# Performance work log

Measured on AMD Instinct MI355X. Metric: run time of the kernel, lower is better.

## Reference

```python
import jax, jax.numpy as jnp
import numpy as np


def setup_inputs() -> dict:
    key = jax.random.key(0)
    ks = jax.random.split(key, 5)
    B, Td, Te, D, U = 8, 64, 1024, 256, 128
    scale = 1.0 / np.sqrt(D)
    return {
        "decoder_output": jax.random.normal(ks[0], (B, Td, D), jnp.float32),
        "encoder_output": jax.random.normal(ks[1], (B, Te, D), jnp.float32),
        "W1": jax.random.normal(ks[2], (D, U), jnp.float32) * scale,
        "b1": jnp.zeros((U,), jnp.float32),
        "W2": jax.random.normal(ks[3], (D, U), jnp.float32) * scale,
        "b2": jnp.zeros((U,), jnp.float32),
        "V": jax.random.normal(ks[4], (U, 1), jnp.float32) * (1.0 / np.sqrt(U)),
        "bV": jnp.zeros((1,), jnp.float32),
    }


def reference(decoder_output, encoder_output, W1, b1, W2, b2, V, bV):
    # Original loops over decoder timesteps (state unused) -> fully vectorized.
    # w_enc: [B,Te,U] computed ONCE (original wastefully recomputes per step;
    # math is identical).
    w_enc = jnp.einsum("bsd,du->bsu", encoder_output, W1) + b1
    w_dec = jnp.einsum("btd,du->btu", decoder_output, W2) + b2
    # additive score: [B,Td,Te]
    score = (
        jnp.einsum("btsu,u->bts", jnp.tanh(w_enc[:, None, :, :] + w_dec[:, :, None, :]), V[:, 0])
        + bV[0]
    )
    attn = jax.nn.softmax(score, axis=-1)  # softmax over encoder time
    context = jnp.einsum("bts,bsd->btd", attn, encoder_output)  # [B,Td,D]
    return context
```

## Files before the change

### kernel.cpp

```cpp
#include <hip/hip_runtime.h>
#include <math.h>

#define NB   8
#define TD   64
#define TE   1024
#define DDIM 256
#define UDIM 128

__device__ __forceinline__ float rcp_fast(float x) {
    return __builtin_amdgcn_rcpf(x);
}

__global__ __launch_bounds__(256) void k_compute_E(
    const float* __restrict__ enc, const float* __restrict__ dec,
    const float* __restrict__ W1, const float* __restrict__ b1,
    const float* __restrict__ W2, const float* __restrict__ b2,
    float* __restrict__ E_enc, float* __restrict__ E_dec)
{
    __shared__ alignas(16) float ldsT[DDIM][20];

    const int blk = blockIdx.x;
    const float *W, *bias, *in;
    float *out;
    if (blk < 512) {
        in   = enc + (size_t)blk * 16 * DDIM;
        W    = W1;  bias = b1;
        out  = E_enc + (size_t)blk * 16 * UDIM;
    } else {
        const int bd = blk - 512;
        in   = dec + (size_t)bd * 16 * DDIM;
        W    = W2;  bias = b2;
        out  = E_dec + (size_t)bd * 16 * UDIM;
    }

    const int tid = threadIdx.x;
    for (int i = tid; i < 16 * DDIM; i += 256) {
        const int r = i >> 8;
        const int d = i & 255;
        ldsT[d][r] = in[i];
    }
    __syncthreads();

    const int u0 = (tid & 63) * 2;
    const int r0 = (tid >> 6) * 4;

    float acc[4][2];
    #pragma unroll
    for (int r = 0; r < 4; ++r) { acc[r][0] = 0.f; acc[r][1] = 0.f; }

    #pragma unroll 4
    for (int d = 0; d < DDIM; ++d) {
        const float2 w2 = *(const float2*)(W + d * UDIM + u0);
        const float4 a4 = *(const float4*)(&ldsT[d][r0]);
        acc[0][0] = fmaf(a4.x, w2.x, acc[0][0]); acc[0][1] = fmaf(a4.x, w2.y, acc[0][1]);
        acc[1][0] = fmaf(a4.y, w2.x, acc[1][0]); acc[1][1] = fmaf(a4.y, w2.y, acc[1][1]);
        acc[2][0] = fmaf(a4.z, w2.x, acc[2][0]); acc[2][1] = fmaf(a4.z, w2.y, acc[2][1]);
        acc[3][0] = fmaf(a4.w, w2.x, acc[3][0]); acc[3][1] = fmaf(a4.w, w2.y, acc[3][1]);
    }

    const float k2l2e = 2.0f * 1.4426950408889634f;
    const float bb0 = bias[u0], bb1 = bias[u0 + 1];
    #pragma unroll
    for (int r = 0; r < 4; ++r) {
        const float e0 = exp2f((acc[r][0] + bb0) * k2l2e);
        const float e1 = exp2f((acc[r][1] + bb1) * k2l2e);
        *(float2*)(out + (size_t)(r0 + r) * UDIM + u0) = make_float2(e0, e1);
    }
}

__global__ __launch_bounds__(1024) void k_fused(
    const float* __restrict__ E_enc, const float* __restrict__ E_dec,
    const float* __restrict__ V, const float* __restrict__ enc,
    float* __restrict__ out)
{
    __shared__ alignas(16) float pa[TE];
    __shared__ alignas(16) float pb[TE];
    __shared__ alignas(16) float red[8][2][DDIM];
    __shared__ float redm[16][2];
    __shared__ float reds[16][2];

    const int blk = blockIdx.x;
    const int b   = blk >> 5;
    const int t0  = (blk & 31) * 2;
    const int tid = threadIdx.x;

    const float* er0 = E_dec + (size_t)(b * TD + t0) * UDIM;
    const float* er1 = er0 + UDIM;

    const int s = tid;
    const float* erow = E_enc + (size_t)(b * TE + s) * UDIM;

    float acc0 = 0.f, acc1 = 0.f;
    #pragma unroll 8
    for (int u = 0; u < UDIM; u += 4) {
        const float4 e  = *(const float4*)(erow + u);
        const float4 a0 = *(const float4*)(er0 + u);
        const float4 a1 = *(const float4*)(er1 + u);
        const float4 vv = *(const float4*)(V + u);
        acc0 = fmaf(vv.x, rcp_fast(fmaf(e.x, a0.x, 1.f)), acc0);
        acc1 = fmaf(vv.x, rcp_fast(fmaf(e.x, a1.x, 1.f)), acc1);
        acc0 = fmaf(vv.y, rcp_fast(fmaf(e.y, a0.y, 1.f)), acc0);
        acc1 = fmaf(vv.y, rcp_fast(fmaf(e.y, a1.y, 1.f)), acc1);
        acc0 = fmaf(vv.z, rcp_fast(fmaf(e.z, a0.z, 1.f)), acc0);
        acc1 = fmaf(vv.z, rcp_fast(fmaf(e.z, a1.z, 1.f)), acc1);
        acc0 = fmaf(vv.w, rcp_fast(fmaf(e.w, a0.w, 1.f)), acc0);
        acc1 = fmaf(vv.w, rcp_fast(fmaf(e.w, a1.w, 1.f)), acc1);
    }
    acc0 *= -2.0f;
    acc1 *= -2.0f;

    float m0 = acc0, m1 = acc1;
    #pragma unroll
    for (int off = 32; off; off >>= 1) {
        m0 = fmaxf(m0, __shfl_xor(m0, off));
        m1 = fmaxf(m1, __shfl_xor(m1, off));
    }
    const int wv = tid >> 6;
    if ((tid & 63) == 0) { redm[wv][0] = m0; redm[wv][1] = m1; }
    __syncthreads();
    float gm0 = -3.4e38f, gm1 = -3.4e38f;
    #pragma unroll
    for (int i = 0; i < 16; ++i) {
        gm0 = fmaxf(gm0, redm[i][0]);
        gm1 = fmaxf(gm1, redm[i][1]);
    }

    const float p0 = __expf(acc0 - gm0);
    const float p1 = __expf(acc1 - gm1);

    float s0 = p0, s1 = p1;
    #pragma unroll
    for (int off = 32; off; off >>= 1) {
        s0 += __shfl_xor(s0, off);
        s1 += __shfl_xor(s1, off);
    }
    if ((tid & 63) == 0) { reds[wv][0] = s0; reds[wv][1] = s1; }
    __syncthreads();
    float gs0 = 0.f, gs1 = 0.f;
    #pragma unroll
    for (int i = 0; i < 16; ++i) { gs0 += reds[i][0]; gs1 += reds[i][1]; }

    pa[s] = p0 * rcp_fast(gs0);
    pb[s] = p1 * rcp_fast(gs1);
    __syncthreads();

    const int dp = tid & 127;
    const int d0 = dp * 2;
    const int sq = tid >> 7;
    const float* ebase = enc + ((size_t)(b * TE + sq * 128)) * DDIM + d0;

    float c00 = 0.f, c01 = 0.f, c10 = 0.f, c11 = 0.f;
    #pragma unroll 4
    for (int ss = 0; ss < 128; ++ss) {
        const float a0 = pa[sq * 128 + ss];
        const float a1 = pb[sq * 128 + ss];
        const float2 e = *(const float2*)(ebase + (size_t)ss * DDIM);
        c00 = fmaf(a0, e.x, c00);
        c01 = fmaf(a0, e.y, c01);
        c10 = fmaf(a1, e.x, c10);
        c11 = fmaf(a1, e.y, c11);
    }
    *(float2*)(&red[sq][0][d0]) = make_float2(c00, c01);
    *(float2*)(&red[sq][1][d0]) = make_float2(c10, c11);
    __syncthreads();

    if (tid < 512) {
        const int t = tid >> 8;
        const int d = tid & 255;
        float r = 0.f;
        #pragma unroll
        for (int q = 0; q < 8; ++q) r += red[q][t][d];
        out[(size_t)(b * TD + t0 + t) * DDIM + d] = r;
    }
}

extern "C" void kernel_launch(void* const* d_in, const int* in_sizes, int n_in,
                              void* d_out, int out_size, void* d_ws, size_t ws_size,
                              hipStream_t stream) {
    const float* dec = (const float*)d_in[0];
    const float* enc = (const float*)d_in[1];
    const float* W1  = (const float*)d_in[2];
    const float* b1  = (const float*)d_in[3];
    const float* W2  = (const float*)d_in[4];
    const float* b2  = (const float*)d_in[5];
    const float* V   = (const float*)d_in[6];

    float* ws    = (float*)d_ws;
    float* E_enc = ws;
    float* E_dec = E_enc + (size_t)NB * TE * UDIM;

    k_compute_E<<<544, 256,  0, stream>>>(enc, dec, W1, b1, W2, b2, E_enc, E_dec);
    k_fused    <<<256, 1024, 0, stream>>>(E_enc, E_dec, V, enc, (float*)d_out);
}
```

Baseline: 131.1 us.

## Split attention over encoder chunks with flash-style partial softmax and combine kernel

Restructures the fused score/softmax/context kernel so each block handles 16 decoder steps over a 128-long encoder chunk, instead of 2 decoder steps over the full encoder length. Each block writes partial max/sum and partial context, and a new combine kernel merges them with rescaling. The encoder projection is stored in a float4-interleaved transposed layout so loads across encoder positions coalesce, and each encoder tile is reused across more decoder rows. The cost is an extra kernel launch and a global round trip for the partial results.

```diff
diff --git a/kernel.cpp b/kernel.cpp
--- a/kernel.cpp
+++ b/kernel.cpp
@@ -6,6 +6,10 @@
 #define TE   1024
 #define DDIM 256
 #define UDIM 128
+#define NSG  8
+#define SLEN 128
+#define NTG  4
+#define TLEN 16
 
 __device__ __forceinline__ float rcp_fast(float x) {
     return __builtin_amdgcn_rcpf(x);
@@ -15,163 +19,195 @@
     const float* __restrict__ enc, const float* __restrict__ dec,
     const float* __restrict__ W1, const float* __restrict__ b1,
     const float* __restrict__ W2, const float* __restrict__ b2,
-    float* __restrict__ E_enc, float* __restrict__ E_dec)
+    float* __restrict__ E_T, float* __restrict__ E_dec)
 {
     __shared__ alignas(16) float ldsT[DDIM][20];
 
     const int blk = blockIdx.x;
-    const float *W, *bias, *in;
-    float *out;
+    const int tid = threadIdx.x;
+    const float k2l2e = 2.0f * 1.4426950408889634f;
+
     if (blk < 512) {
-        in   = enc + (size_t)blk * 16 * DDIM;
-        W    = W1;  bias = b1;
-        out  = E_enc + (size_t)blk * 16 * UDIM;
+        const int b    = blk >> 6;
+        const int row0 = (blk & 63) * 16;
+        const float* in = enc + ((size_t)b * TE + row0) * DDIM;
+
+        for (int i = tid; i < 16 * DDIM; i += 256) {
+            ldsT[i & 255][i >> 8] = in[i];
+        }
+        __syncthreads();
+
+        const int uq = tid >> 3;
+        const int rr = (tid & 7) * 2;
+        const int u0 = uq * 4;
+
+        float4 A0 = make_float4(0.f, 0.f, 0.f, 0.f);
+        float4 A1 = make_float4(0.f, 0.f, 0.f, 0.f);
+
+        #pragma unroll 8
+        for (int d = 0; d < DDIM; ++d) {
+            const float4 w4 = *(const float4*)(W1 + d * UDIM + u0);
+            const float2 a2 = *(const float2*)(&ldsT[d][rr]);
+            A0.x = fmaf(a2.x, w4.x, A0.x); A1.x = fmaf(a2.y, w4.x, A1.x);
+            A0.y = fmaf(a2.x, w4.y, A0.y); A1.y = fmaf(a2.y, w4.y, A1.y);
+            A0.z = fmaf(a2.x, w4.z, A0.z); A1.z = fmaf(a2.y, w4.z, A1.z);
+            A0.w = fmaf(a2.x, w4.w, A0.w); A1.w = fmaf(a2.y, w4.w, A1.w);
+        }
+
+        const float4 bb = *(const float4*)(b1 + u0);
+        float4 q0, q1;
+        q0.x = exp2f((A0.x + bb.x) * k2l2e);  q1.x = exp2f((A1.x + bb.x) * k2l2e);
+        q0.y = exp2f((A0.y + bb.y) * k2l2e);  q1.y = exp2f((A1.y + bb.y) * k2l2e);
+        q0.z = exp2f((A0.z + bb.z) * k2l2e);  q1.z = exp2f((A1.z + bb.z) * k2l2e);
+        q0.w = exp2f((A0.w + bb.w) * k2l2e);  q1.w = exp2f((A1.w + bb.w) * k2l2e);
+
+        float4* E_T4 = (float4*)E_T;
+        const size_t qbase = ((size_t)b * 32 + uq) * TE + row0 + rr;
+        E_T4[qbase]     = q0;
+        E_T4[qbase + 1] = q1;
     } else {
         const int bd = blk - 512;
-        in   = dec + (size_t)bd * 16 * DDIM;
-        W    = W2;  bias = b2;
-        out  = E_dec + (size_t)bd * 16 * UDIM;
-    }
-
+        const float* in = dec + (size_t)bd * 16 * DDIM;
+        float* out = E_dec + (size_t)bd * 16 * UDIM;
+
+        for (int i = tid; i < 16 * DDIM; i += 256) {
+            ldsT[i & 255][i >> 8] = in[i];
+        }
+        __syncthreads();
+
+        const int u0 = (tid & 63) * 2;
+        const int r0 = (tid >> 6) * 4;
+
+        float acc[4][2];
+        #pragma unroll
+        for (int r = 0; r < 4; ++r) { acc[r][0] = 0.f; acc[r][1] = 0.f; }
+
+        #pragma unroll 8
+        for (int d = 0; d < DDIM; ++d) {
+            const float2 w2 = *(const float2*)(W2 + d * UDIM + u0);
+            const float4 a4 = *(const float4*)(&ldsT[d][r0]);
+            acc[0][0] = fmaf(a4.x, w2.x, acc[0][0]); acc[0][1] = fmaf(a4.x, w2.y, acc[0][1]);
+            acc[1][0] = fmaf(a4.y, w2.x, acc[1][0]); acc[1][1] = fmaf(a4.y, w2.y, acc[1][1]);
+            acc[2][0] = fmaf(a4.z, w2.x, acc[2][0]); acc[2][1] = fmaf(a4.z, w2.y, acc[2][1]);
+            acc[3][0] = fmaf(a4.w, w2.x, acc[3][0]); acc[3][1] = fmaf(a4.w, w2.y, acc[3][1]);
+        }
+
+        const float bb0 = b2[u0], bb1 = b2[u0 + 1];
+        #pragma unroll
+        for (int r = 0; r < 4; ++r) {
+            const float e0 = exp2f((acc[r][0] + bb0) * k2l2e);
+            const float e1 = exp2f((acc[r][1] + bb1) * k2l2e);
+            *(float2*)(out + (size_t)(r0 + r) * UDIM + u0) = make_float2(e0, e1);
+        }
+    }
+}
+
+__global__ __launch_bounds__(1024) void k_fused2(
+    const float* __restrict__ E_T, const float* __restrict__ E_dec,
+    const float* __restrict__ V, const float* __restrict__ enc,
+    float2* __restrict__ ml, float* __restrict__ part)
+{
+    __shared__ float sc[TLEN][SLEN];
+
+    const int blk = blockIdx.x;
+    const int b   = blk >> 5;
+    const int tg  = (blk >> 3) & 3;
+    const int sg  = blk & 7;
     const int tid = threadIdx.x;
-    for (int i = tid; i < 16 * DDIM; i += 256) {
-        const int r = i >> 8;
-        const int d = i & 255;
-        ldsT[d][r] = in[i];
-    }
+
+    const int sl = tid & 127;
+    const int th = __builtin_amdgcn_readfirstlane(tid >> 7);
+    const int sglob = sg * SLEN + sl;
+
+    const float4* e4  = (const float4*)E_T + (size_t)b * 32 * TE + sglob;
+    const float*  er0 = E_dec + (size_t)(b * TD + tg * TLEN + th) * UDIM;
+    const float*  er1 = er0 + 8 * UDIM;
+
+    float acc0 = 0.f, acc1 = 0.f;
+    #pragma unroll 8
+    for (int uq = 0; uq < 32; ++uq) {
+        const float4 e = e4[(size_t)uq * TE];
+        const int u0 = uq * 4;
+        const float v0 = V[u0], v1 = V[u0+1], v2 = V[u0+2], v3 = V[u0+3];
+        acc0 = fmaf(v0, rcp_fast(fmaf(e.x, er0[u0  ], 1.f)), acc0);
+        acc1 = fmaf(v0, rcp_fast(fmaf(e.x, er1[u0  ], 1.f)), acc1);
+        acc0 = fmaf(v1, rcp_fast(fmaf(e.y, er0[u0+1], 1.f)), acc0);
+        acc1 = fmaf(v1, rcp_fast(fmaf(e.y, er1[u0+1], 1.f)), acc1);
+        acc0 = fmaf(v2, rcp_fast(fmaf(e.z, er0[u0+2], 1.f)), acc0);
+        acc1 = fmaf(v2, rcp_fast(fmaf(e.z, er1[u0+2], 1.f)), acc1);
+        acc0 = fmaf(v3, rcp_fast(fmaf(e.w, er0[u0+3], 1.f)), acc0);
+        acc1 = fmaf(v3, rcp_fast(fmaf(e.w, er1[u0+3], 1.f)), acc1);
+    }
+    sc[th][sl]     = -2.0f * acc0;
+    sc[th + 8][sl] = -2.0f * acc1;
     __syncthreads();
 
-    const int u0 = (tid & 63) * 2;
-    const int r0 = (tid >> 6) * 4;
-
-    float acc[4][2];
-    #pragma unroll
-    for (int r = 0; r < 4; ++r) { acc[r][0] = 0.f; acc[r][1] = 0.f; }
-
+    const int tw = __builtin_amdgcn_readfirstlane(tid >> 6);
+    const int ln = tid & 63;
+    const float v0s = sc[tw][ln];
+    const float v1s = sc[tw][ln + 64];
+    float m = fmaxf(v0s, v1s);
+    #pragma unroll
+    for (int off = 32; off; off >>= 1) m = fmaxf(m, __shfl_xor(m, off));
+    const float p0 = __expf(v0s - m);
+    const float p1 = __expf(v1s - m);
+    float l = p0 + p1;
+    #pragma unroll
+    for (int off = 32; off; off >>= 1) l += __shfl_xor(l, off);
+    sc[tw][ln]      = p0;
+    sc[tw][ln + 64] = p1;
+    if (ln == 0)
+        ml[(size_t)(b * TD + tg * TLEN + tw) * NSG + sg] = make_float2(m, l);
+    __syncthreads();
+
+    const int dp = tid & 127;  const int d0 = dp * 2;
+    const int tq = __builtin_amdgcn_readfirstlane(tid >> 7);
+    const float* eb = enc + ((size_t)(b * TE + sg * SLEN)) * DDIM + d0;
+
+    float c00 = 0.f, c01 = 0.f, c10 = 0.f, c11 = 0.f;
     #pragma unroll 4
-    for (int d = 0; d < DDIM; ++d) {
-        const float2 w2 = *(const float2*)(W + d * UDIM + u0);
-        const float4 a4 = *(const float4*)(&ldsT[d][r0]);
-        acc[0][0] = fmaf(a4.x, w2.x, acc[0][0]); acc[0][1] = fmaf(a4.x, w2.y, acc[0][1]);
-        acc[1][0] = fmaf(a4.y, w2.x, acc[1][0]); acc[1][1] = fmaf(a4.y, w2.y, acc[1][1]);
-        acc[2][0] = fmaf(a4.z, w2.x, acc[2][0]); acc[2][1] = fmaf(a4.z, w2.y, acc[2][1]);
-        acc[3][0] = fmaf(a4.w, w2.x, acc[3][0]); acc[3][1] = fmaf(a4.w, w2.y, acc[3][1]);
-    }
-
-    const float k2l2e = 2.0f * 1.4426950408889634f;
-    const float bb0 = bias[u0], bb1 = bias[u0 + 1];
-    #pragma unroll
-    for (int r = 0; r < 4; ++r) {
-        const float e0 = exp2f((acc[r][0] + bb0) * k2l2e);
-        const float e1 = exp2f((acc[r][1] + bb1) * k2l2e);
-        *(float2*)(out + (size_t)(r0 + r) * UDIM + u0) = make_float2(e0, e1);
-    }
-}
-
-__global__ __launch_bounds__(1024) void k_fused(
-    const float* __restrict__ E_enc, const float* __restrict__ E_dec,
-    const float* __restrict__ V, const float* __restrict__ enc,
+    for (int s = 0; s < SLEN; ++s) {
+        const float2 e = *(const float2*)(eb + (size_t)s * DDIM);
+        const float a0 = sc[tq * 2][s];
+        const float a1 = sc[tq * 2 + 1][s];
+        c00 = fmaf(a0, e.x, c00); c01 = fmaf(a0, e.y, c01);
+        c10 = fmaf(a1, e.x, c10); c11 = fmaf(a1, e.y, c11);
+    }
+    const int trow = tg * TLEN + tq * 2;
+    float* pb = part + (((size_t)(b * NSG + sg) * TD) + trow) * DDIM + d0;
+    *(float2*)pb          = make_float2(c00, c01);
+    *(float2*)(pb + DDIM) = make_float2(c10, c11);
+}
+
+__global__ __launch_bounds__(256) void k_combine(
+    const float2* __restrict__ ml, const float* __restrict__ part,
     float* __restrict__ out)
 {
-    __shared__ alignas(16) float pa[TE];
-    __shared__ alignas(16) float pb[TE];
-    __shared__ alignas(16) float red[8][2][DDIM];
-    __shared__ float redm[16][2];
-    __shared__ float reds[16][2];
-
-    const int blk = blockIdx.x;
-    const int b   = blk >> 5;
-    const int t0  = (blk & 31) * 2;
-    const int tid = threadIdx.x;
-
-    const float* er0 = E_dec + (size_t)(b * TD + t0) * UDIM;
-    const float* er1 = er0 + UDIM;
-
-    const int s = tid;
-    const float* erow = E_enc + (size_t)(b * TE + s) * UDIM;
-
-    float acc0 = 0.f, acc1 = 0.f;
-    #pragma unroll 8
-    for (int u = 0; u < UDIM; u += 4) {
-        const float4 e  = *(const float4*)(erow + u);
-        const float4 a0 = *(const float4*)(er0 + u);
-        const float4 a1 = *(const float4*)(er1 + u);
-        const float4 vv = *(const float4*)(V + u);
-        acc0 = fmaf(vv.x, rcp_fast(fmaf(e.x, a0.x, 1.f)), acc0);
-        acc1 = fmaf(vv.x, rcp_fast(fmaf(e.x, a1.x, 1.f)), acc1);
-        acc0 = fmaf(vv.y, rcp_fast(fmaf(e.y, a0.y, 1.f)), acc0);
-        acc1 = fmaf(vv.y, rcp_fast(fmaf(e.y, a1.y, 1.f)), acc1);
-        acc0 = fmaf(vv.z, rcp_fast(fmaf(e.z, a0.z, 1.f)), acc0);
-        acc1 = fmaf(vv.z, rcp_fast(fmaf(e.z, a1.z, 1.f)), acc1);
-        acc0 = fmaf(vv.w, rcp_fast(fmaf(e.w, a0.w, 1.f)), acc0);
-        acc1 = fmaf(vv.w, rcp_fast(fmaf(e.w, a1.w, 1.f)), acc1);
-    }
-    acc0 *= -2.0f;
-    acc1 *= -2.0f;
-
-    float m0 = acc0, m1 = acc1;
-    #pragma unroll
-    for (int off = 32; off; off >>= 1) {
-        m0 = fmaxf(m0, __shfl_xor(m0, off));
-        m1 = fmaxf(m1, __shfl_xor(m1, off));
-    }
-    const int wv = tid >> 6;
-    if ((tid & 63) == 0) { redm[wv][0] = m0; redm[wv][1] = m1; }
-    __syncthreads();
-    float gm0 = -3.4e38f, gm1 = -3.4e38f;
-    #pragma unroll
-    for (int i = 0; i < 16; ++i) {
-        gm0 = fmaxf(gm0, redm[i][0]);
-        gm1 = fmaxf(gm1, redm[i][1]);
-    }
-
-    const float p0 = __expf(acc0 - gm0);
-    const float p1 = __expf(acc1 - gm1);
-
-    float s0 = p0, s1 = p1;
-    #pragma unroll
-    for (int off = 32; off; off >>= 1) {
-        s0 += __shfl_xor(s0, off);
-        s1 += __shfl_xor(s1, off);
-    }
-    if ((tid & 63) == 0) { reds[wv][0] = s0; reds[wv][1] = s1; }
-    __syncthreads();
-    float gs0 = 0.f, gs1 = 0.f;
-    #pragma unroll
-    for (int i = 0; i < 16; ++i) { gs0 += reds[i][0]; gs1 += reds[i][1]; }
-
-    pa[s] = p0 * rcp_fast(gs0);
-    pb[s] = p1 * rcp_fast(gs1);
-    __syncthreads();
-
-    const int dp = tid & 127;
-    const int d0 = dp * 2;
-    const int sq = tid >> 7;
-    const float* ebase = enc + ((size_t)(b * TE + sq * 128)) * DDIM + d0;
-
-    float c00 = 0.f, c01 = 0.f, c10 = 0.f, c11 = 0.f;
-    #pragma unroll 4
-    for (int ss = 0; ss < 128; ++ss) {
-        const float a0 = pa[sq * 128 + ss];
-        const float a1 = pb[sq * 128 + ss];
-        const float2 e = *(const float2*)(ebase + (size_t)ss * DDIM);
-        c00 = fmaf(a0, e.x, c00);
-        c01 = fmaf(a0, e.y, c01);
-        c10 = fmaf(a1, e.x, c10);
-        c11 = fmaf(a1, e.y, c11);
-    }
-    *(float2*)(&red[sq][0][d0]) = make_float2(c00, c01);
-    *(float2*)(&red[sq][1][d0]) = make_float2(c10, c11);
-    __syncthreads();
-
-    if (tid < 512) {
-        const int t = tid >> 8;
-        const int d = tid & 255;
-        float r = 0.f;
-        #pragma unroll
-        for (int q = 0; q < 8; ++q) r += red[q][t][d];
-        out[(size_t)(b * TD + t0 + t) * DDIM + d] = r;
-    }
+    const int bt = blockIdx.x;
+    const int d  = threadIdx.x;
+    const int b  = bt >> 6, t = bt & 63;
+
+    float2 mls[NSG];
+    float m_g = -3.4e38f;
+    #pragma unroll
+    for (int sg = 0; sg < NSG; ++sg) {
+        mls[sg] = ml[(size_t)bt * NSG + sg];
+        m_g = fmaxf(m_g, mls[sg].x);
+    }
+    float l_g = 0.f;
+    float w[NSG];
+    #pragma unroll
+    for (int sg = 0; sg < NSG; ++sg) {
+        w[sg] = __expf(mls[sg].x - m_g);
+        l_g = fmaf(mls[sg].y, w[sg], l_g);
+    }
+    const float inv = rcp_fast(l_g);
+
+    float r = 0.f;
+    #pragma unroll
+    for (int sg = 0; sg < NSG; ++sg)
+        r = fmaf(part[(((size_t)(b * NSG + sg) * TD) + t) * DDIM + d], w[sg], r);
+    out[(size_t)bt * DDIM + d] = r * inv;
 }
 
 extern "C" void kernel_launch(void* const* d_in, const int* in_sizes, int n_in,
@@ -185,10 +221,13 @@
     const float* b2  = (const float*)d_in[5];
     const float* V   = (const float*)d_in[6];
 
-    float* ws    = (float*)d_ws;
-    float* E_enc = ws;
-    float* E_dec = E_enc + (size_t)NB * TE * UDIM;
-
-    k_compute_E<<<544, 256,  0, stream>>>(enc, dec, W1, b1, W2, b2, E_enc, E_dec);
-    k_fused    <<<256, 1024, 0, stream>>>(E_enc, E_dec, V, enc, (float*)d_out);
-}
+    float*  ws    = (float*)d_ws;
+    float*  E_T   = ws;
+    float*  E_dec = E_T + (size_t)NB * UDIM * TE;
+    float2* ml    = (float2*)(E_dec + (size_t)512 * UDIM);
+    float*  part  = (float*)(ml + (size_t)NB * TD * NSG);
+
+    k_compute_E<<<544, 256,  0, stream>>>(enc, dec, W1, b1, W2, b2, E_T, E_dec);
+    k_fused2   <<<256, 1024, 0, stream>>>(E_T, E_dec, V, enc, ml, part);
+    k_combine  <<<512, 256,  0, stream>>>(ml, part, (float*)d_out);
+}
```

Result: no change. 131.1 us (+0.0%).
